# Optimization experiments

Hardware: AMD Instinct MI355X
Metric: run time of the kernel (lower is better)

Reference implementation:

```python
import jax, jax.numpy as jnp
import numpy as np


def quantize_ternary(w):
    # BitNet b1.58: scale by mean |w|, round, clamp to {-1,0,1}
    gamma = jnp.maximum(jnp.mean(jnp.abs(w)), 1e-8)
    return jnp.clip(jnp.round(w / gamma), -1.0, 1.0)


def setup_inputs() -> dict:
    key = jax.random.key(0)
    k1, k2, k3 = jax.random.split(key, 3)
    in_features, out_features = 4096, 4096
    x = jax.random.normal(k1, (4, 2048, in_features), dtype=jnp.float32)
    # kaiming_uniform-like init
    bound_w = 1.0 / np.sqrt(in_features)
    weight = jax.random.uniform(k2, (out_features, in_features), dtype=jnp.float32,
                                minval=-bound_w * np.sqrt(3.0), maxval=bound_w * np.sqrt(3.0))
    bias = jax.random.uniform(k3, (out_features,), dtype=jnp.float32,
                              minval=-bound_w, maxval=bound_w)
    return {"x": x, "weight": weight, "bias": bias}


def reference(x, weight, bias):
    qw = quantize_ternary(weight)  # [out, in], values in {-1,0,1}
    # F.linear: x @ qw.T + bias
    return jnp.einsum('bsi,oi->bso', x, qw) + bias
```

## Files before the change

kernel.cpp:

```cpp
#include <hip/hip_runtime.h>
#include <stdint.h>

#define M_DIM 8192
#define N_DIM 4096
#define K_DIM 4096
#define BM 128
#define BN 128
#define BK 128

typedef int i32x4 __attribute__((ext_vector_type(4)));

__device__ __forceinline__ void async_copy16(const void* g, void* l) {
    __builtin_amdgcn_global_load_lds(
        (const __attribute__((address_space(1))) void*)g,
        (__attribute__((address_space(3))) void*)l, 16, 0, 0);
}

__global__ __launch_bounds__(256) void abssum_partial(const float4* __restrict__ w,
                                                      double* __restrict__ partials) {
    const int lane = threadIdx.x & 63;
    const int wave = threadIdx.x >> 6;
    int base = blockIdx.x * 4096 + threadIdx.x;
    float s = 0.f;
    #pragma unroll
    for (int i = 0; i < 16; i++) {
        float4 v = w[base + i * 256];
        s += fabsf(v.x) + fabsf(v.y) + fabsf(v.z) + fabsf(v.w);
    }
    double d = (double)s;
    #pragma unroll
    for (int off = 32; off > 0; off >>= 1) d += __shfl_down(d, off, 64);
    __shared__ double wsum[4];
    if (lane == 0) wsum[wave] = d;
    __syncthreads();
    if (threadIdx.x == 0)
        partials[blockIdx.x] = (wsum[0] + wsum[1]) + (wsum[2] + wsum[3]);
}

__global__ __launch_bounds__(256) void gamma_reduce(const double* __restrict__ partials,
                                                    float* __restrict__ gamma_out) {
    const int lane = threadIdx.x & 63;
    const int wave = threadIdx.x >> 6;
    double d = partials[threadIdx.x] + partials[threadIdx.x + 256] +
               partials[threadIdx.x + 512] + partials[threadIdx.x + 768];
    #pragma unroll
    for (int off = 32; off > 0; off >>= 1) d += __shfl_down(d, off, 64);
    __shared__ double wsum[4];
    if (lane == 0) wsum[wave] = d;
    __syncthreads();
    if (threadIdx.x == 0) {
        double total = (wsum[0] + wsum[1]) + (wsum[2] + wsum[3]);
        float g = (float)(total * (1.0 / 16777216.0));
        gamma_out[0] = fmaxf(g, 1e-8f);
    }
}

__global__ __launch_bounds__(256) void wquant(const float4* __restrict__ w,
                                              char4* __restrict__ qw,
                                              const float* __restrict__ gamma_p, int n4) {
    float gamma = gamma_p[0];
    int i = blockIdx.x * blockDim.x + threadIdx.x;
    if (i >= n4) return;
    float4 v = w[i];
    char4 o;
    o.x = (signed char)fminf(fmaxf(rintf(v.x / gamma), -1.f), 1.f);
    o.y = (signed char)fminf(fmaxf(rintf(v.y / gamma), -1.f), 1.f);
    o.z = (signed char)fminf(fmaxf(rintf(v.z / gamma), -1.f), 1.f);
    o.w = (signed char)fminf(fmaxf(rintf(v.w / gamma), -1.f), 1.f);
    qw[i] = o;
}

__global__ __launch_bounds__(256) void xquant(const float4* __restrict__ x,
                                              char4* __restrict__ xq,
                                              float* __restrict__ xscale) {
    const int row = blockIdx.x;
    const int lane = threadIdx.x & 63;
    const int wave = threadIdx.x >> 6;
    const float4* xr = x + (size_t)row * (K_DIM / 4);
    float4 v[4];
    float m = 0.f;
    #pragma unroll
    for (int i = 0; i < 4; i++) {
        v[i] = xr[threadIdx.x + i * 256];
        m = fmaxf(m, fmaxf(fmaxf(fabsf(v[i].x), fabsf(v[i].y)),
                           fmaxf(fabsf(v[i].z), fabsf(v[i].w))));
    }
    #pragma unroll
    for (int off = 32; off > 0; off >>= 1) m = fmaxf(m, __shfl_down(m, off, 64));
    __shared__ float wmax[4];
    if (lane == 0) wmax[wave] = m;
    __syncthreads();
    const float mx = fmaxf(fmaxf(wmax[0], wmax[1]), fmaxf(wmax[2], wmax[3]));
    const float scale = fmaxf(mx * (1.f / 127.f), 1e-30f);
    const float inv = 1.f / scale;
    if (threadIdx.x == 0) xscale[row] = scale;
    char4* oq = xq + (size_t)row * (K_DIM / 4);
    #pragma unroll
    for (int i = 0; i < 4; i++) {
        char4 o;
        o.x = (signed char)fminf(fmaxf(rintf(v[i].x * inv), -127.f), 127.f);
        o.y = (signed char)fminf(fmaxf(rintf(v[i].y * inv), -127.f), 127.f);
        o.z = (signed char)fminf(fmaxf(rintf(v[i].z * inv), -127.f), 127.f);
        o.w = (signed char)fminf(fmaxf(rintf(v[i].w * inv), -127.f), 127.f);
        oq[threadIdx.x + i * 256] = o;
    }
}

__global__ __launch_bounds__(256) void gemm_kernel(
    const char* __restrict__ xq,
    const char* __restrict__ qw,
    const float* __restrict__ xscale,
    const float* __restrict__ bias,
    float* __restrict__ out)
{
    __shared__ __align__(16) char As[BM * BK];
    __shared__ __align__(16) char Bs[BN * BK];

    const int tid  = threadIdx.x;
    const int wave = tid >> 6;
    const int lane = tid & 63;
    const int wm   = (wave >> 1) * 64;
    const int wn   = (wave & 1) * 64;
    const int lm   = lane & 15;
    const int quad = lane >> 4;

    const int bm = blockIdx.y * BM;
    const int bn = blockIdx.x * BN;

    const int sub = lane >> 3;
    const int ch  = (lane & 7) ^ sub;
    const int seg0 = wave * 4;

    const char* gA[4];
    const char* gB[4];
    #pragma unroll
    for (int i = 0; i < 4; i++) {
        const int r = (seg0 + i) * 8 + sub;
        gA[i] = xq + (size_t)(bm + r) * K_DIM + ch * 16;
        gB[i] = qw + (size_t)(bn + r) * K_DIM + ch * 16;
    }

    i32x4 acc[4][4];
    #pragma unroll
    for (int i = 0; i < 4; i++)
        #pragma unroll
        for (int j = 0; j < 4; j++) acc[i][j] = (i32x4){0, 0, 0, 0};

    for (int kt = 0; kt < K_DIM; kt += BK) {
        #pragma unroll
        for (int i = 0; i < 4; i++) {
            async_copy16(gA[i] + kt, &As[(seg0 + i) * 1024]);
            async_copy16(gB[i] + kt, &Bs[(seg0 + i) * 1024]);
        }
        __syncthreads();

        #pragma unroll
        for (int ks = 0; ks < 2; ks++) {
            const int p = ((ks * 4 + quad) ^ (lm & 7)) * 16;
            i32x4 a[4], b[4];
            #pragma unroll
            for (int mi = 0; mi < 4; mi++)
                a[mi] = *(const i32x4*)&As[(wm + mi * 16 + lm) * BK + p];
            #pragma unroll
            for (int ni = 0; ni < 4; ni++)
                b[ni] = *(const i32x4*)&Bs[(wn + ni * 16 + lm) * BK + p];

            #pragma unroll
            for (int mi = 0; mi < 4; mi++)
                #pragma unroll
                for (int ni = 0; ni < 4; ni++)
                    acc[mi][ni] = __builtin_amdgcn_mfma_i32_16x16x64_i8(
                        a[mi], b[ni], acc[mi][ni], 0, 0, 0);
        }
        __syncthreads();
    }

    float bl[4];
    #pragma unroll
    for (int ni = 0; ni < 4; ni++) bl[ni] = bias[bn + wn + ni * 16 + lm];

    #pragma unroll
    for (int mi = 0; mi < 4; mi++) {
        #pragma unroll
        for (int r = 0; r < 4; r++) {
            const int grow = bm + wm + mi * 16 + quad * 4 + r;
            const float sc = xscale[grow];
            float* orow = out + (size_t)grow * N_DIM + bn;
            #pragma unroll
            for (int ni = 0; ni < 4; ni++)
                orow[wn + ni * 16 + lm] = sc * (float)acc[mi][ni][r] + bl[ni];
        }
    }
}

extern "C" void kernel_launch(void* const* d_in, const int* in_sizes, int n_in,
                              void* d_out, int out_size, void* d_ws, size_t ws_size,
                              hipStream_t stream) {
    const float* x    = (const float*)d_in[0];
    const float* w    = (const float*)d_in[1];
    const float* bias = (const float*)d_in[2];
    float* out = (float*)d_out;

    char* ws = (char*)d_ws;
    char*   xq       = ws;
    char*   qw       = ws + (size_t)M_DIM * K_DIM;
    float*  xscale   = (float*)(qw + (size_t)N_DIM * K_DIM);
    double* partials = (double*)(xscale + M_DIM);
    float*  gamma_p  = (float*)(partials + 1024);

    const int wn4 = (N_DIM * K_DIM) / 4;

    abssum_partial<<<1024, 256, 0, stream>>>((const float4*)w, partials);
    gamma_reduce<<<1, 256, 0, stream>>>(partials, gamma_p);
    wquant<<<(wn4 + 255) / 256, 256, 0, stream>>>((const float4*)w, (char4*)qw, gamma_p, wn4);
    xquant<<<M_DIM, 256, 0, stream>>>((const float4*)x, (char4*)xq, xscale);

    dim3 grid(N_DIM / BN, M_DIM / BM);
    gemm_kernel<<<grid, 256, 0, stream>>>(xq, qw, xscale, bias, out);
}
```

Baseline: 412.7 us.

## Rewrite int8 GEMM as 256x256 tile with 4-slot async LDS pipeline

The int8 MFMA GEMM moves from 128x128 tiles with one synchronous stage to 256x256 tiles with 512 threads and a 4-slot ring buffer of 64-wide K slabs. Global-to-LDS async loads run three slabs ahead, with waits done through explicit vmcnt counts. Each slab is split into two MFMA phases interleaved with the loads and barriers, and s_setprio is raised during compute. The larger tile cuts global traffic per output, and the deeper pipeline hides load latency. In exchange it needs more registers and LDS per block and relies on hand-counted vmcnt ordering, which is fragile.

```diff
diff --git a/kernel.cpp b/kernel.cpp
--- a/kernel.cpp
+++ b/kernel.cpp
@@ -4,9 +4,11 @@
 #define M_DIM 8192
 #define N_DIM 4096
 #define K_DIM 4096
-#define BM 128
-#define BN 128
-#define BK 128
+#define BM 256
+#define BN 256
+#define BKS 64
+#define NSLAB (K_DIM / BKS)
+#define SLOT_BYTES (256 * BKS)
 
 typedef int i32x4 __attribute__((ext_vector_type(4)));
 
@@ -106,89 +108,130 @@
     }
 }
 
-__global__ __launch_bounds__(256) void gemm_kernel(
+__global__ __launch_bounds__(512, 2) void gemm_kernel(
     const char* __restrict__ xq,
     const char* __restrict__ qw,
     const float* __restrict__ xscale,
     const float* __restrict__ bias,
     float* __restrict__ out)
 {
-    __shared__ __align__(16) char As[BM * BK];
-    __shared__ __align__(16) char Bs[BN * BK];
+    __shared__ __align__(16) char As[4][SLOT_BYTES];
+    __shared__ __align__(16) char Bs[4][SLOT_BYTES];
 
     const int tid  = threadIdx.x;
     const int wave = tid >> 6;
     const int lane = tid & 63;
-    const int wm   = (wave >> 1) * 64;
-    const int wn   = (wave & 1) * 64;
+    const int wm   = (wave >> 2) * 128;
+    const int wn   = (wave & 3) * 64;
     const int lm   = lane & 15;
-    const int quad = lane >> 4;
+    const int q4   = lane >> 4;
 
     const int bm = blockIdx.y * BM;
     const int bn = blockIdx.x * BN;
 
-    const int sub = lane >> 3;
-    const int ch  = (lane & 7) ^ sub;
-    const int seg0 = wave * 4;
-
-    const char* gA[4];
-    const char* gB[4];
-    #pragma unroll
-    for (int i = 0; i < 4; i++) {
-        const int r = (seg0 + i) * 8 + sub;
-        gA[i] = xq + (size_t)(bm + r) * K_DIM + ch * 16;
-        gB[i] = qw + (size_t)(bn + r) * K_DIM + ch * 16;
-    }
-
-    i32x4 acc[4][4];
-    #pragma unroll
-    for (int i = 0; i < 4; i++)
+    const int rsub = lane >> 2;
+    const int csw  = (lane & 3) ^ ((lane >> 3) & 3);
+    const char* gA[2];
+    const char* gB[2];
+    int ldsOff[2];
+    #pragma unroll
+    for (int j = 0; j < 2; j++) {
+        const int r = wave * 32 + j * 16 + rsub;
+        gA[j] = xq + (size_t)(bm + r) * K_DIM + csw * 16;
+        gB[j] = qw + (size_t)(bn + r) * K_DIM + csw * 16;
+        ldsOff[j] = (wave * 32 + j * 16) * BKS;
+    }
+
+    i32x4 acc[8][4];
+    #pragma unroll
+    for (int i = 0; i < 8; i++)
         #pragma unroll
         for (int j = 0; j < 4; j++) acc[i][j] = (i32x4){0, 0, 0, 0};
 
-    for (int kt = 0; kt < K_DIM; kt += BK) {
-        #pragma unroll
-        for (int i = 0; i < 4; i++) {
-            async_copy16(gA[i] + kt, &As[(seg0 + i) * 1024]);
-            async_copy16(gB[i] + kt, &Bs[(seg0 + i) * 1024]);
-        }
-        __syncthreads();
-
-        #pragma unroll
-        for (int ks = 0; ks < 2; ks++) {
-            const int p = ((ks * 4 + quad) ^ (lm & 7)) * 16;
-            i32x4 a[4], b[4];
-            #pragma unroll
-            for (int mi = 0; mi < 4; mi++)
-                a[mi] = *(const i32x4*)&As[(wm + mi * 16 + lm) * BK + p];
+    const int pc = (q4 ^ ((lm >> 1) & 3)) * 16;
+
+    #pragma unroll
+    for (int s = 0; s < 3; s++) {
+        #pragma unroll
+        for (int j = 0; j < 2; j++) {
+            async_copy16(gA[j] + s * BKS, &As[s][ldsOff[j]]);
+            async_copy16(gB[j] + s * BKS, &Bs[s][ldsOff[j]]);
+        }
+    }
+    asm volatile("s_waitcnt vmcnt(8)" ::: "memory");
+    __builtin_amdgcn_s_barrier();
+
+    for (int t = 0; t < NSLAB; ++t) {
+        const char* Ab = As[t & 3];
+        const char* Bb = Bs[t & 3];
+        const int  ts       = t + 3;
+        const bool do_stage = ts < NSLAB;
+        const int  slot     = ts & 3;
+
+        i32x4 a[4], b[4];
+        #pragma unroll
+        for (int mi = 0; mi < 4; mi++)
+            a[mi] = *(const i32x4*)(Ab + (wm + mi * 16 + lm) * BKS + pc);
+        #pragma unroll
+        for (int ni = 0; ni < 4; ni++)
+            b[ni] = *(const i32x4*)(Bb + (wn + ni * 16 + lm) * BKS + pc);
+        if (do_stage) {
+            async_copy16(gA[0] + ts * BKS, &As[slot][ldsOff[0]]);
+            async_copy16(gB[0] + ts * BKS, &Bs[slot][ldsOff[0]]);
+        }
+        __builtin_amdgcn_s_barrier();
+        __builtin_amdgcn_s_setprio(1);
+        #pragma unroll
+        for (int mi = 0; mi < 4; mi++)
             #pragma unroll
             for (int ni = 0; ni < 4; ni++)
-                b[ni] = *(const i32x4*)&Bs[(wn + ni * 16 + lm) * BK + p];
-
-            #pragma unroll
-            for (int mi = 0; mi < 4; mi++)
-                #pragma unroll
-                for (int ni = 0; ni < 4; ni++)
-                    acc[mi][ni] = __builtin_amdgcn_mfma_i32_16x16x64_i8(
-                        a[mi], b[ni], acc[mi][ni], 0, 0, 0);
-        }
-        __syncthreads();
-    }
-
-    float bl[4];
-    #pragma unroll
-    for (int ni = 0; ni < 4; ni++) bl[ni] = bias[bn + wn + ni * 16 + lm];
-
-    #pragma unroll
-    for (int mi = 0; mi < 4; mi++) {
-        #pragma unroll
-        for (int r = 0; r < 4; r++) {
-            const int grow = bm + wm + mi * 16 + quad * 4 + r;
-            const float sc = xscale[grow];
-            float* orow = out + (size_t)grow * N_DIM + bn;
+                acc[mi][ni] = __builtin_amdgcn_mfma_i32_16x16x64_i8(
+                    a[mi], b[ni], acc[mi][ni], 0, 0, 0);
+        __builtin_amdgcn_s_setprio(0);
+        __builtin_amdgcn_s_barrier();
+
+        i32x4 a2[4];
+        #pragma unroll
+        for (int mi = 0; mi < 4; mi++)
+            a2[mi] = *(const i32x4*)(Ab + (wm + (4 + mi) * 16 + lm) * BKS + pc);
+        if (do_stage) {
+            async_copy16(gA[1] + ts * BKS, &As[slot][ldsOff[1]]);
+            async_copy16(gB[1] + ts * BKS, &Bs[slot][ldsOff[1]]);
+        }
+        __builtin_amdgcn_s_barrier();
+        __builtin_amdgcn_s_setprio(1);
+        #pragma unroll
+        for (int mi = 0; mi < 4; mi++)
             #pragma unroll
             for (int ni = 0; ni < 4; ni++)
-                orow[wn + ni * 16 + lm] = sc * (float)acc[mi][ni][r] + bl[ni];
+                acc[4 + mi][ni] = __builtin_amdgcn_mfma_i32_16x16x64_i8(
+                    a2[mi], b[ni], acc[4 + mi][ni], 0, 0, 0);
+        __builtin_amdgcn_s_setprio(0);
+
+        if (t < NSLAB - 3) {
+            asm volatile("s_waitcnt vmcnt(8)" ::: "memory");
+        } else if (t == NSLAB - 3) {
+            asm volatile("s_waitcnt vmcnt(4)" ::: "memory");
+        } else if (t == NSLAB - 2) {
+            asm volatile("s_waitcnt vmcnt(0)" ::: "memory");
+        }
+        if (t < NSLAB - 1) __builtin_amdgcn_s_barrier();
+    }
+
+    float bl[4];
+    #pragma unroll
+    for (int ni = 0; ni < 4; ni++) bl[ni] = bias[bn + wn + ni * 16 + lm];
+
+    #pragma unroll
+    for (int mi = 0; mi < 8; mi++) {
+        #pragma unroll
+        for (int r = 0; r < 4; r++) {
+            const int grow = bm + wm + mi * 16 + q4 * 4 + r;
+            const float sc = xscale[grow];
+            float* orow = out + (size_t)grow * N_DIM + bn + wn;
+            #pragma unroll
+            for (int ni = 0; ni < 4; ni++)
+                orow[ni * 16 + lm] = sc * (float)acc[mi][ni][r] + bl[ni];
         }
     }
 }
@@ -216,5 +259,5 @@
     xquant<<<M_DIM, 256, 0, stream>>>((const float4*)x, (char4*)xq, xscale);
 
     dim3 grid(N_DIM / BN, M_DIM / BM);
-    gemm_kernel<<<grid, 256, 0, stream>>>(xq, qw, xscale, bias, out);
-}
+    gemm_kernel<<<grid, 512, 0, stream>>>(xq, qw, xscale, bias, out);
+}
```

Result: no change. 407.8 us (-1.2%).
